# Performance work log

Hardware: AMD Instinct MI355X
Metric: run time of the kernel (lower is better)

The kernel has to match this reference:

```python
import jax, jax.numpy as jnp
import numpy as np

ALPHA = 1.702
LIMIT = 7.0


def setup_inputs() -> dict:
    key = jax.random.key(0)
    ks = jax.random.split(key, 6)
    B, T, H, I, E = 2, 1024, 2048, 2048, 8
    hidden_states = jax.random.normal(ks[0], (B, T, H), dtype=jnp.float32)
    routing_weights = jax.random.uniform(ks[1], (B * T, E), dtype=jnp.float32)
    routing_weights = routing_weights / routing_weights.sum(-1, keepdims=True)
    gate_up_proj = jax.random.normal(ks[2], (E, H, 2 * I), dtype=jnp.float32) * 0.02
    gate_up_proj_bias = jax.random.normal(ks[3], (E, 2 * I), dtype=jnp.float32) * 0.02
    down_proj = jax.random.normal(ks[4], (E, I, H), dtype=jnp.float32) * 0.02
    down_proj_bias = jax.random.normal(ks[5], (E, H), dtype=jnp.float32) * 0.02
    return {
        "hidden_states": hidden_states,
        "routing_weights": routing_weights,
        "gate_up_proj": gate_up_proj,
        "gate_up_proj_bias": gate_up_proj_bias,
        "down_proj": down_proj,
        "down_proj_bias": down_proj_bias,
    }


def reference(hidden_states, routing_weights, gate_up_proj, gate_up_proj_bias,
              down_proj, down_proj_bias):
    # Inference branch of GptOssExperts: dense repeat-all-experts grouped GEMM
    B, T, H = hidden_states.shape
    x = hidden_states.reshape(-1, H)                      # [N, H]
    # [E, N, 2I]
    gate_up = jnp.einsum('nh,ehd->end', x, gate_up_proj) + gate_up_proj_bias[:, None, :]
    gate = gate_up[..., ::2]                              # interleaved split
    up = gate_up[..., 1::2]
    gate = jnp.minimum(gate, LIMIT)
    up = jnp.clip(up, -LIMIT, LIMIT)
    glu = gate * jax.nn.sigmoid(gate * ALPHA)
    # [E, N, H]
    out = jnp.einsum('eni,eih->enh', (up + 1.0) * glu, down_proj) + down_proj_bias[:, None, :]
    out = out * routing_weights.T[..., None]              # weight per (expert, token)
    return out.sum(axis=0).reshape(B, T, H)
```

## Files before the change

### kernel.cpp

```cpp
#include <hip/hip_runtime.h>
#include <cstdint>
#include <cstddef>

#define ALPHA 1.702f
#define LIMIT 7.0f

#define NTOK 2048
#define HDIM 2048
#define IDIM 2048
#define I2   4096
#define NEXP 8

typedef float f32x4 __attribute__((ext_vector_type(4)));
typedef short bf16x8 __attribute__((ext_vector_type(8)));
typedef unsigned short u16;

__device__ __forceinline__ u16 f2bf(float f) {
  unsigned u = __float_as_uint(f);
  u += 0x7fffu + ((u >> 16) & 1u);
  return (u16)(u >> 16);
}

__device__ __forceinline__ void gload_lds16(const void* g, void* l) {
  __builtin_amdgcn_global_load_lds(
      (const __attribute__((address_space(1))) void*)g,
      (__attribute__((address_space(3))) void*)l, 16, 0, 0);
}

#define BARRIER() do { asm volatile("" ::: "memory"); __builtin_amdgcn_s_barrier(); asm volatile("" ::: "memory"); } while (0)
#define VMCNT(n)  asm volatile("s_waitcnt vmcnt(" #n ")" ::: "memory")

__global__ __launch_bounds__(256) void k_cvt(const float* __restrict__ in,
                                             u16* __restrict__ out) {
  int i = blockIdx.x * blockDim.x + threadIdx.x;
  const float4* p = (const float4*)in + (size_t)i * 2;
  float4 a = p[0], b = p[1];
  union { u16 s[8]; uint4 v; } o;
  o.s[0] = f2bf(a.x); o.s[1] = f2bf(a.y); o.s[2] = f2bf(a.z); o.s[3] = f2bf(a.w);
  o.s[4] = f2bf(b.x); o.s[5] = f2bf(b.y); o.s[6] = f2bf(b.z); o.s[7] = f2bf(b.w);
  ((uint4*)out)[i] = o.v;
}

__global__ __launch_bounds__(256) void k_tc(const float* __restrict__ in,
                                            u16* __restrict__ out, int R, int C) {
  __shared__ float tile[32][33];
  const size_t mo = (size_t)blockIdx.z * R * C;
  const float* ip = in + mo;
  u16* op = out + mo;
  int c0 = blockIdx.x * 32, r0 = blockIdx.y * 32;
  int t = threadIdx.x;
  int tr = t >> 3, tc = (t & 7) * 4;
  float4 v = *(const float4*)&ip[(size_t)(r0 + tr) * C + c0 + tc];
  tile[tr][tc] = v.x; tile[tr][tc + 1] = v.y;
  tile[tr][tc + 2] = v.z; tile[tr][tc + 3] = v.w;
  __syncthreads();
  ushort4 o;
  o.x = f2bf(tile[tc + 0][tr]);
  o.y = f2bf(tile[tc + 1][tr]);
  o.z = f2bf(tile[tc + 2][tr]);
  o.w = f2bf(tile[tc + 3][tr]);
  *(ushort4*)&op[(size_t)(c0 + tr) * R + r0 + tc] = o;
}

#define MFMA_Q(mh, nh, bb) \
  _Pragma("unroll") for (int mm = 0; mm < 4; ++mm) \
  _Pragma("unroll") for (int nn = 0; nn < 2; ++nn) \
  _Pragma("unroll") for (int ks = 0; ks < 2; ++ks) \
    acc[(mh)*4+mm][(nh)*2+nn] = __builtin_amdgcn_mfma_f32_16x16x32_bf16( \
        a[mm][ks], (bb)[nn][ks], acc[(mh)*4+mm][(nh)*2+nn], 0, 0, 0);

__global__ __launch_bounds__(512, 2) void k_gemm1(const u16* __restrict__ xbf,
                                                  const u16* __restrict__ w1t,
                                                  const float* __restrict__ gub,
                                                  const float* __restrict__ rw,
                                                  u16* __restrict__ inter) {
  __shared__ __align__(16) u16 Als[4][128 * 64];
  __shared__ __align__(16) u16 Bls[4][128 * 64];

  const int bid = (int)blockIdx.x;
  const int L = (bid & 7) * 128 + (bid >> 3);
  const int mtile = L & 7, ntile = (L >> 3) & 15, e = L >> 7;
  const int row0 = mtile * 256, col0 = ntile * 256;
  const u16* A = xbf;
  const u16* B = w1t + (size_t)e * I2 * HDIM;

  const int tid = threadIdx.x;
  const int w = tid >> 6, lane = tid & 63;
  const int wr = w >> 2, wc = w & 3;
  const int rrow = lane & 15, klane = lane >> 4;
  const int sA = (wr * 64 + rrow) * 64;
  const int sB = (wc * 32 + rrow) * 64;
  int kofs[2];
  kofs[0] = ((klane ^ (rrow & 7)) << 3);
  kofs[1] = (((4 + klane) ^ (rrow & 7)) << 3);

  auto stA = [&](int reg, int h, int k0) {
#pragma unroll
    for (int j = 0; j < 2; ++j) {
      int c = (w * 2 + j) * 64 + lane;
      int r = c >> 3, gg = c & 7;
      int ksw = ((gg ^ (r & 7)) << 3);
      int R = ((r >> 6) << 7) + h * 64 + (r & 63);
      gload_lds16(A + (size_t)(row0 + R) * HDIM + k0 + ksw,
                  &Als[reg][(size_t)(w * 2 + j) * 512]);
    }
  };
  auto stB = [&](int reg, int h, int k0) {
#pragma unroll
    for (int j = 0; j < 2; ++j) {
      int c = (w * 2 + j) * 64 + lane;
      int r = c >> 3, gg = c & 7;
      int ksw = ((gg ^ (r & 7)) << 3);
      int C = ((r >> 5) << 6) + h * 32 + (r & 31);
      gload_lds16(B + (size_t)(col0 + C) * HDIM + k0 + ksw,
                  &Bls[reg][(size_t)(w * 2 + j) * 512]);
    }
  };

  f32x4 acc[8][4];
#pragma unroll
  for (int i = 0; i < 8; ++i)
#pragma unroll
    for (int j = 0; j < 4; ++j) acc[i][j] = (f32x4){0.f, 0.f, 0.f, 0.f};

  bf16x8 a[4][2], b0[2][2], b1[2][2];
  auto rdA = [&](int reg) {
#pragma unroll
    for (int mm = 0; mm < 4; ++mm)
#pragma unroll
      for (int ks = 0; ks < 2; ++ks)
        a[mm][ks] = *(const bf16x8*)&Als[reg][sA + mm * 1024 + kofs[ks]];
  };
  auto rdB0 = [&](int reg) {
#pragma unroll
    for (int nn = 0; nn < 2; ++nn)
#pragma unroll
      for (int ks = 0; ks < 2; ++ks)
        b0[nn][ks] = *(const bf16x8*)&Bls[reg][sB + nn * 1024 + kofs[ks]];
  };
  auto rdB1 = [&](int reg) {
#pragma unroll
    for (int nn = 0; nn < 2; ++nn)
#pragma unroll
      for (int ks = 0; ks < 2; ++ks)
        b1[nn][ks] = *(const bf16x8*)&Bls[reg][sB + nn * 1024 + kofs[ks]];
  };

  stB(0, 0, 0); stB(1, 1, 0); stA(0, 0, 0); stA(1, 1, 0);
  stB(2, 0, 64); stB(3, 1, 64); stA(2, 0, 64);
  VMCNT(6);
  BARRIER();

  for (int t = 0; t < 32; ++t) {
    const int b = t & 1;
    const int kA1 = (t + 1 < 32 ? t + 1 : 31) * 64;
    const int kN  = (t + 2 < 32 ? t + 2 : 31) * 64;
    const int rA1 = 2 * ((t + 1) & 1) + 1;

    rdA(2 * b); rdB0(2 * b); rdB1(2 * b + 1);
    stA(rA1, 1, kA1);
    BARRIER();
    __builtin_amdgcn_s_setprio(1);
    MFMA_Q(0, 0, b0); MFMA_Q(0, 1, b1);
    __builtin_amdgcn_s_setprio(0);
    BARRIER();

    rdA(2 * b + 1);
    stB(2 * b, 0, kN); stB(2 * b + 1, 1, kN); stA(2 * b, 0, kN);
    BARRIER();
    __builtin_amdgcn_s_setprio(1);
    MFMA_Q(1, 0, b0); MFMA_Q(1, 1, b1);
    __builtin_amdgcn_s_setprio(0);
    VMCNT(6);
    BARRIER();
  }

  const float* bias = gub + (size_t)e * I2;
  u16* ip = inter + (size_t)e * NTOK * IDIM;
#pragma unroll
  for (int ai = 0; ai < 8; ++ai) {
    const int mh = ai >> 2, mm = ai & 3;
#pragma unroll
    for (int bj = 0; bj < 4; ++bj) {
      const int nh = bj >> 1, nn = bj & 1;
      const int col = col0 + wc * 64 + nh * 32 + nn * 16 + rrow;
      const float bv = bias[col];
#pragma unroll
      for (int r = 0; r < 4; ++r) {
        const int row = row0 + wr * 128 + mh * 64 + mm * 16 + klane * 4 + r;
        float gu = acc[ai][bj][r] + bv;
        float pg = __shfl_xor(gu, 1);
        float gate = (lane & 1) ? pg : gu;
        float up   = (lane & 1) ? gu : pg;
        gate = fminf(gate, LIMIT);
        up = fminf(fmaxf(up, -LIMIT), LIMIT);
        float glu = gate / (1.f + __expf(-ALPHA * gate));
        float val = (up + 1.f) * glu * rw[row * NEXP + e];
        if (!(lane & 1)) ip[(size_t)row * IDIM + (col >> 1)] = f2bf(val);
      }
    }
  }
}

__global__ __launch_bounds__(512, 2) void k_gemm2(const u16* __restrict__ inter,
                                                  const u16* __restrict__ w2t,
                                                  float* __restrict__ part) {
  __shared__ __align__(16) u16 Als[4][128 * 64];
  __shared__ __align__(16) u16 Bls[4][128 * 64];

  const int bid = (int)blockIdx.x;
  const int L = (bid & 7) * 32 + (bid >> 3);
  const int mtile = L & 7, ntile = (L >> 3) & 7, sp = L >> 6;
  const int row0 = mtile * 256, col0 = ntile * 256;
  const int es = sp * 2;

  const int tid = threadIdx.x;
  const int w = tid >> 6, lane = tid & 63;
  const int wr = w >> 2, wc = w & 3;
  const int rrow = lane & 15, klane = lane >> 4;
  const int sA = (wr * 64 + rrow) * 64;
  const int sB = (wc * 32 + rrow) * 64;
  int kofs[2];
  kofs[0] = ((klane ^ (rrow & 7)) << 3);
  kofs[1] = (((4 + klane) ^ (rrow & 7)) << 3);

  auto stA = [&](int reg, int h, int k0) {
    const u16* Ab = inter + (size_t)(es + (k0 >> 11)) * NTOK * IDIM;
    const int kk = k0 & 2047;
#pragma unroll
    for (int j = 0; j < 2; ++j) {
      int c = (w * 2 + j) * 64 + lane;
      int r = c >> 3, gg = c & 7;
      int ksw = ((gg ^ (r & 7)) << 3);
      int R = ((r >> 6) << 7) + h * 64 + (r & 63);
      gload_lds16(Ab + (size_t)(row0 + R) * IDIM + kk + ksw,
                  &Als[reg][(size_t)(w * 2 + j) * 512]);
    }
  };
  auto stB = [&](int reg, int h, int k0) {
    const u16* Bb = w2t + (size_t)(es + (k0 >> 11)) * HDIM * IDIM;
    const int kk = k0 & 2047;
#pragma unroll
    for (int j = 0; j < 2; ++j) {
      int c = (w * 2 + j) * 64 + lane;
      int r = c >> 3, gg = c & 7;
      int ksw = ((gg ^ (r & 7)) << 3);
      int C = ((r >> 5) << 6) + h * 32 + (r & 31);
      gload_lds16(Bb + (size_t)(col0 + C) * IDIM + kk + ksw,
                  &Bls[reg][(size_t)(w * 2 + j) * 512]);
    }
  };

  f32x4 acc[8][4];
#pragma unroll
  for (int i = 0; i < 8; ++i)
#pragma unroll
    for (int j = 0; j < 4; ++j) acc[i][j] = (f32x4){0.f, 0.f, 0.f, 0.f};

  bf16x8 a[4][2], b0[2][2], b1[2][2];
  auto rdA = [&](int reg) {
#pragma unroll
    for (int mm = 0; mm < 4; ++mm)
#pragma unroll
      for (int ks = 0; ks < 2; ++ks)
        a[mm][ks] = *(const bf16x8*)&Als[reg][sA + mm * 1024 + kofs[ks]];
  };
  auto rdB0 = [&](int reg) {
#pragma unroll
    for (int nn = 0; nn < 2; ++nn)
#pragma unroll
      for (int ks = 0; ks < 2; ++ks)
        b0[nn][ks] = *(const bf16x8*)&Bls[reg][sB + nn * 1024 + kofs[ks]];
  };
  auto rdB1 = [&](int reg) {
#pragma unroll
    for (int nn = 0; nn < 2; ++nn)
#pragma unroll
      for (int ks = 0; ks < 2; ++ks)
        b1[nn][ks] = *(const bf16x8*)&Bls[reg][sB + nn * 1024 + kofs[ks]];
  };

  stB(0, 0, 0); stB(1, 1, 0); stA(0, 0, 0); stA(1, 1, 0);
  stB(2, 0, 64); stB(3, 1, 64); stA(2, 0, 64);
  VMCNT(6);
  BARRIER();

  for (int t = 0; t < 64; ++t) {
    const int b = t & 1;
    const int kA1 = (t + 1 < 64 ? t + 1 : 63) * 64;
    const int kN  = (t + 2 < 64 ? t + 2 : 63) * 64;
    const int rA1 = 2 * ((t + 1) & 1) + 1;

    rdA(2 * b); rdB0(2 * b); rdB1(2 * b + 1);
    stA(rA1, 1, kA1);
    BARRIER();
    __builtin_amdgcn_s_setprio(1);
    MFMA_Q(0, 0, b0); MFMA_Q(0, 1, b1);
    __builtin_amdgcn_s_setprio(0);
    BARRIER();

    rdA(2 * b + 1);
    stB(2 * b, 0, kN); stB(2 * b + 1, 1, kN); stA(2 * b, 0, kN);
    BARRIER();
    __builtin_amdgcn_s_setprio(1);
    MFMA_Q(1, 0, b0); MFMA_Q(1, 1, b1);
    __builtin_amdgcn_s_setprio(0);
    VMCNT(6);
    BARRIER();
  }

  float* pp = part + (size_t)sp * NTOK * HDIM;
#pragma unroll
  for (int ai = 0; ai < 8; ++ai) {
    const int mh = ai >> 2, mm = ai & 3;
#pragma unroll
    for (int bj = 0; bj < 4; ++bj) {
      const int nh = bj >> 1, nn = bj & 1;
      const int col = col0 + wc * 64 + nh * 32 + nn * 16 + rrow;
#pragma unroll
      for (int r = 0; r < 4; ++r) {
        const int row = row0 + wr * 128 + mh * 64 + mm * 16 + klane * 4 + r;
        pp[(size_t)row * HDIM + col] = acc[ai][bj][r];
      }
    }
  }
}

__global__ __launch_bounds__(256) void k_reduce(const float* __restrict__ part,
                                                const float* __restrict__ dbias,
                                                const float* __restrict__ rw,
                                                float* __restrict__ out) {
  const int i = blockIdx.x * 256 + threadIdx.x;
  const int i4 = i * 4;
  const int n = i4 >> 11;
  const int h = i4 & 2047;
  const size_t MSZ = (size_t)NTOK * HDIM / 4;
  const float4* p = (const float4*)part;
  float4 v0 = p[i];
  float4 v1 = p[i + MSZ];
  float4 v2 = p[i + 2 * MSZ];
  float4 v3 = p[i + 3 * MSZ];
  float4 s;
  s.x = (v0.x + v1.x) + (v2.x + v3.x);
  s.y = (v0.y + v1.y) + (v2.y + v3.y);
  s.z = (v0.z + v1.z) + (v2.z + v3.z);
  s.w = (v0.w + v1.w) + (v2.w + v3.w);
#pragma unroll
  for (int e = 0; e < NEXP; ++e) {
    float rwe = rw[n * NEXP + e];
    float4 db = *(const float4*)&dbias[(size_t)e * HDIM + h];
    s.x += rwe * db.x; s.y += rwe * db.y;
    s.z += rwe * db.z; s.w += rwe * db.w;
  }
  *(float4*)&out[i4] = s;
}

extern "C" void kernel_launch(void* const* d_in, const int* in_sizes, int n_in,
                              void* d_out, int out_size, void* d_ws, size_t ws_size,
                              hipStream_t stream) {
  const float* hs   = (const float*)d_in[0];
  const float* rw   = (const float*)d_in[1];
  const float* gup  = (const float*)d_in[2];
  const float* gupb = (const float*)d_in[3];
  const float* dwn  = (const float*)d_in[4];
  const float* dwnb = (const float*)d_in[5];
  float* out = (float*)d_out;

  u16* xbf   = (u16*)d_ws;
  u16* w1t   = xbf + (size_t)NTOK * HDIM;
  u16* w2t   = w1t + (size_t)NEXP * I2 * HDIM;
  u16* inter = w2t + (size_t)NEXP * HDIM * IDIM;
  float* part = (float*)w1t;
  size_t need = ((size_t)NTOK * HDIM + (size_t)NEXP * I2 * HDIM +
                 (size_t)NEXP * HDIM * IDIM + (size_t)NEXP * NTOK * IDIM) * 2;
  if (ws_size < need) return;

  k_cvt<<<(NTOK * HDIM) / (256 * 8), 256, 0, stream>>>(hs, xbf);

  dim3 g1(I2 / 32, HDIM / 32, NEXP);
  k_tc<<<g1, 256, 0, stream>>>(gup, w1t, HDIM, I2);
  dim3 g2(HDIM / 32, IDIM / 32, NEXP);
  k_tc<<<g2, 256, 0, stream>>>(dwn, w2t, IDIM, HDIM);

  k_gemm1<<<dim3(1024), 512, 0, stream>>>(xbf, w1t, gupb, rw, inter);

  k_gemm2<<<dim3(256), 512, 0, stream>>>(inter, w2t, part);

  k_reduce<<<dim3(NTOK * HDIM / 1024), 256, 0, stream>>>(part, dwnb, rw, out);
}
```

Measured before the change: 591.5 us.

## Simplify GEMM main loop to single-phase double-buffered load/compute

Replaces the two-phase interleaved ping-pong schedule, where loads of one half-tile overlapped MFMAs on the other half, with a simpler loop per K step. Each step reads all A/B fragments from LDS, runs all 64 MFMAs, then issues the global-to-LDS loads for step t+2 and waits. The idea is fewer barriers and a longer uninterrupted MFMA burst per iteration. In exchange it raises register pressure (a[8][2] plus bb[4][2] held at once) and loses the fine-grained overlap of loads with compute inside a step.

```diff
diff --git a/kernel.cpp b/kernel.cpp
--- a/kernel.cpp
+++ b/kernel.cpp
@@ -62,12 +62,6 @@
   *(ushort4*)&op[(size_t)(c0 + tr) * R + r0 + tc] = o;
 }
 
-#define MFMA_Q(mh, nh, bb) \
-  _Pragma("unroll") for (int mm = 0; mm < 4; ++mm) \
-  _Pragma("unroll") for (int nn = 0; nn < 2; ++nn) \
-  _Pragma("unroll") for (int ks = 0; ks < 2; ++ks) \
-    acc[(mh)*4+mm][(nh)*2+nn] = __builtin_amdgcn_mfma_f32_16x16x32_bf16( \
-        a[mm][ks], (bb)[nn][ks], acc[(mh)*4+mm][(nh)*2+nn], 0, 0, 0);
 
 __global__ __launch_bounds__(512, 2) void k_gemm1(const u16* __restrict__ xbf,
                                                   const u16* __restrict__ w1t,
@@ -88,8 +82,6 @@
   const int w = tid >> 6, lane = tid & 63;
   const int wr = w >> 2, wc = w & 3;
   const int rrow = lane & 15, klane = lane >> 4;
-  const int sA = (wr * 64 + rrow) * 64;
-  const int sB = (wc * 32 + rrow) * 64;
   int kofs[2];
   kofs[0] = ((klane ^ (rrow & 7)) << 3);
   kofs[1] = (((4 + klane) ^ (rrow & 7)) << 3);
@@ -123,72 +115,56 @@
 #pragma unroll
     for (int j = 0; j < 4; ++j) acc[i][j] = (f32x4){0.f, 0.f, 0.f, 0.f};
 
-  bf16x8 a[4][2], b0[2][2], b1[2][2];
-  auto rdA = [&](int reg) {
-#pragma unroll
-    for (int mm = 0; mm < 4; ++mm)
-#pragma unroll
-      for (int ks = 0; ks < 2; ++ks)
-        a[mm][ks] = *(const bf16x8*)&Als[reg][sA + mm * 1024 + kofs[ks]];
-  };
-  auto rdB0 = [&](int reg) {
-#pragma unroll
-    for (int nn = 0; nn < 2; ++nn)
-#pragma unroll
-      for (int ks = 0; ks < 2; ++ks)
-        b0[nn][ks] = *(const bf16x8*)&Bls[reg][sB + nn * 1024 + kofs[ks]];
-  };
-  auto rdB1 = [&](int reg) {
-#pragma unroll
-    for (int nn = 0; nn < 2; ++nn)
-#pragma unroll
-      for (int ks = 0; ks < 2; ++ks)
-        b1[nn][ks] = *(const bf16x8*)&Bls[reg][sB + nn * 1024 + kofs[ks]];
-  };
-
-  stB(0, 0, 0); stB(1, 1, 0); stA(0, 0, 0); stA(1, 1, 0);
-  stB(2, 0, 64); stB(3, 1, 64); stA(2, 0, 64);
-  VMCNT(6);
+  stA(0, 0, 0); stA(1, 1, 0); stB(0, 0, 0); stB(1, 1, 0);
+  stA(2, 0, 64); stA(3, 1, 64); stB(2, 0, 64); stB(3, 1, 64);
+  VMCNT(8);
   BARRIER();
 
   for (int t = 0; t < 32; ++t) {
     const int b = t & 1;
-    const int kA1 = (t + 1 < 32 ? t + 1 : 31) * 64;
-    const int kN  = (t + 2 < 32 ? t + 2 : 31) * 64;
-    const int rA1 = 2 * ((t + 1) & 1) + 1;
-
-    rdA(2 * b); rdB0(2 * b); rdB1(2 * b + 1);
-    stA(rA1, 1, kA1);
-    BARRIER();
+    bf16x8 a[8][2], bb[4][2];
+#pragma unroll
+    for (int m = 0; m < 8; ++m)
+#pragma unroll
+      for (int ks = 0; ks < 2; ++ks)
+        a[m][ks] = *(const bf16x8*)&Als[2 * b + (m >> 2)]
+                       [(wr * 64 + (m & 3) * 16 + rrow) * 64 + kofs[ks]];
+#pragma unroll
+    for (int n = 0; n < 4; ++n)
+#pragma unroll
+      for (int ks = 0; ks < 2; ++ks)
+        bb[n][ks] = *(const bf16x8*)&Bls[2 * b + (n >> 1)]
+                        [(wc * 32 + (n & 1) * 16 + rrow) * 64 + kofs[ks]];
     __builtin_amdgcn_s_setprio(1);
-    MFMA_Q(0, 0, b0); MFMA_Q(0, 1, b1);
+#pragma unroll
+    for (int ks = 0; ks < 2; ++ks)
+#pragma unroll
+      for (int m = 0; m < 8; ++m)
+#pragma unroll
+        for (int n = 0; n < 4; ++n)
+          acc[m][n] = __builtin_amdgcn_mfma_f32_16x16x32_bf16(a[m][ks], bb[n][ks], acc[m][n], 0, 0, 0);
     __builtin_amdgcn_s_setprio(0);
     BARRIER();
 
-    rdA(2 * b + 1);
-    stB(2 * b, 0, kN); stB(2 * b + 1, 1, kN); stA(2 * b, 0, kN);
-    BARRIER();
-    __builtin_amdgcn_s_setprio(1);
-    MFMA_Q(1, 0, b0); MFMA_Q(1, 1, b1);
-    __builtin_amdgcn_s_setprio(0);
-    VMCNT(6);
+    const int kN = (t + 2 < 32 ? t + 2 : 31) * 64;
+    stA(2 * b, 0, kN); stA(2 * b + 1, 1, kN);
+    stB(2 * b, 0, kN); stB(2 * b + 1, 1, kN);
+    VMCNT(8);
     BARRIER();
   }
 
   const float* bias = gub + (size_t)e * I2;
   u16* ip = inter + (size_t)e * NTOK * IDIM;
 #pragma unroll
-  for (int ai = 0; ai < 8; ++ai) {
-    const int mh = ai >> 2, mm = ai & 3;
-#pragma unroll
-    for (int bj = 0; bj < 4; ++bj) {
-      const int nh = bj >> 1, nn = bj & 1;
-      const int col = col0 + wc * 64 + nh * 32 + nn * 16 + rrow;
+  for (int m = 0; m < 8; ++m) {
+#pragma unroll
+    for (int n = 0; n < 4; ++n) {
+      const int col = col0 + wc * 64 + n * 16 + rrow;
       const float bv = bias[col];
 #pragma unroll
       for (int r = 0; r < 4; ++r) {
-        const int row = row0 + wr * 128 + mh * 64 + mm * 16 + klane * 4 + r;
-        float gu = acc[ai][bj][r] + bv;
+        const int row = row0 + wr * 128 + m * 16 + klane * 4 + r;
+        float gu = acc[m][n][r] + bv;
         float pg = __shfl_xor(gu, 1);
         float gate = (lane & 1) ? pg : gu;
         float up   = (lane & 1) ? gu : pg;
@@ -218,8 +194,6 @@
   const int w = tid >> 6, lane = tid & 63;
   const int wr = w >> 2, wc = w & 3;
   const int rrow = lane & 15, klane = lane >> 4;
-  const int sA = (wr * 64 + rrow) * 64;
-  const int sB = (wc * 32 + rrow) * 64;
   int kofs[2];
   kofs[0] = ((klane ^ (rrow & 7)) << 3);
   kofs[1] = (((4 + klane) ^ (rrow & 7)) << 3);
@@ -257,70 +231,54 @@
 #pragma unroll
     for (int j = 0; j < 4; ++j) acc[i][j] = (f32x4){0.f, 0.f, 0.f, 0.f};
 
-  bf16x8 a[4][2], b0[2][2], b1[2][2];
-  auto rdA = [&](int reg) {
-#pragma unroll
-    for (int mm = 0; mm < 4; ++mm)
-#pragma unroll
-      for (int ks = 0; ks < 2; ++ks)
-        a[mm][ks] = *(const bf16x8*)&Als[reg][sA + mm * 1024 + kofs[ks]];
-  };
-  auto rdB0 = [&](int reg) {
-#pragma unroll
-    for (int nn = 0; nn < 2; ++nn)
-#pragma unroll
-      for (int ks = 0; ks < 2; ++ks)
-        b0[nn][ks] = *(const bf16x8*)&Bls[reg][sB + nn * 1024 + kofs[ks]];
-  };
-  auto rdB1 = [&](int reg) {
-#pragma unroll
-    for (int nn = 0; nn < 2; ++nn)
-#pragma unroll
-      for (int ks = 0; ks < 2; ++ks)
-        b1[nn][ks] = *(const bf16x8*)&Bls[reg][sB + nn * 1024 + kofs[ks]];
-  };
-
-  stB(0, 0, 0); stB(1, 1, 0); stA(0, 0, 0); stA(1, 1, 0);
-  stB(2, 0, 64); stB(3, 1, 64); stA(2, 0, 64);
-  VMCNT(6);
+  stA(0, 0, 0); stA(1, 1, 0); stB(0, 0, 0); stB(1, 1, 0);
+  stA(2, 0, 64); stA(3, 1, 64); stB(2, 0, 64); stB(3, 1, 64);
+  VMCNT(8);
   BARRIER();
 
   for (int t = 0; t < 64; ++t) {
     const int b = t & 1;
-    const int kA1 = (t + 1 < 64 ? t + 1 : 63) * 64;
-    const int kN  = (t + 2 < 64 ? t + 2 : 63) * 64;
-    const int rA1 = 2 * ((t + 1) & 1) + 1;
-
-    rdA(2 * b); rdB0(2 * b); rdB1(2 * b + 1);
-    stA(rA1, 1, kA1);
-    BARRIER();
+    bf16x8 a[8][2], bb[4][2];
+#pragma unroll
+    for (int m = 0; m < 8; ++m)
+#pragma unroll
+      for (int ks = 0; ks < 2; ++ks)
+        a[m][ks] = *(const bf16x8*)&Als[2 * b + (m >> 2)]
+                       [(wr * 64 + (m & 3) * 16 + rrow) * 64 + kofs[ks]];
+#pragma unroll
+    for (int n = 0; n < 4; ++n)
+#pragma unroll
+      for (int ks = 0; ks < 2; ++ks)
+        bb[n][ks] = *(const bf16x8*)&Bls[2 * b + (n >> 1)]
+                        [(wc * 32 + (n & 1) * 16 + rrow) * 64 + kofs[ks]];
     __builtin_amdgcn_s_setprio(1);
-    MFMA_Q(0, 0, b0); MFMA_Q(0, 1, b1);
+#pragma unroll
+    for (int ks = 0; ks < 2; ++ks)
+#pragma unroll
+      for (int m = 0; m < 8; ++m)
+#pragma unroll
+        for (int n = 0; n < 4; ++n)
+          acc[m][n] = __builtin_amdgcn_mfma_f32_16x16x32_bf16(a[m][ks], bb[n][ks], acc[m][n], 0, 0, 0);
     __builtin_amdgcn_s_setprio(0);
     BARRIER();
 
-    rdA(2 * b + 1);
-    stB(2 * b, 0, kN); stB(2 * b + 1, 1, kN); stA(2 * b, 0, kN);
+    const int kN = (t + 2 < 64 ? t + 2 : 63) * 64;
+    stA(2 * b, 0, kN); stA(2 * b + 1, 1, kN);
+    stB(2 * b, 0, kN); stB(2 * b + 1, 1, kN);
+    VMCNT(8);
     BARRIER();
-    __builtin_amdgcn_s_setprio(1);
-    MFMA_Q(1, 0, b0); MFMA_Q(1, 1, b1);
-    __builtin_amdgcn_s_setprio(0);
-    VMCNT(6);
-    BARRIER();
   }
 
   float* pp = part + (size_t)sp * NTOK * HDIM;
 #pragma unroll
-  for (int ai = 0; ai < 8; ++ai) {
-    const int mh = ai >> 2, mm = ai & 3;
-#pragma unroll
-    for (int bj = 0; bj < 4; ++bj) {
-      const int nh = bj >> 1, nn = bj & 1;
-      const int col = col0 + wc * 64 + nh * 32 + nn * 16 + rrow;
+  for (int m = 0; m < 8; ++m) {
+#pragma unroll
+    for (int n = 0; n < 4; ++n) {
+      const int col = col0 + wc * 64 + n * 16 + rrow;
 #pragma unroll
       for (int r = 0; r < 4; ++r) {
-        const int row = row0 + wr * 128 + mh * 64 + mm * 16 + klane * 4 + r;
-        pp[(size_t)row * HDIM + col] = acc[ai][bj][r];
+        const int row = row0 + wr * 128 + m * 16 + klane * 4 + r;
+        pp[(size_t)row * HDIM + col] = acc[m][n][r];
       }
     }
   }
```

Measured after the change: 640.8 us. 8.3% more time.
